# Kernel optimization log

Measured on AMD Instinct MI355X. Metric: run time of the kernel, lower is better.

## Reference

```python
import jax, jax.numpy as jnp
import numpy as np
from jax import lax

B, DIM, H, W = 16, 256, 64, 64
NH, KD = 8, 16
NH_KD = NH * KD        # 128
DH = 2 * NH_KD         # 256 (attn_ratio=2)
SCALE = KD ** -0.5
PE_LEN = 16


def conv1x1(x, Wt, b):
    # x: [B,Cin,H,W], Wt: [Cout,Cin]
    return jnp.einsum('oi,bihw->bohw', Wt, x) + b[None, :, None, None]


def dwconv3x3(x, Wt, b):
    # depthwise 3x3, pad 1. Wt: [C,1,3,3]
    C = x.shape[1]
    y = lax.conv_general_dilated(x, Wt, window_strides=(1, 1),
                                 padding=((1, 1), (1, 1)),
                                 feature_group_count=C,
                                 dimension_numbers=('NCHW', 'OIHW', 'NCHW'))
    return y + b[None, :, None, None]


def relu6(x):
    return jnp.clip(x, 0.0, 6.0)


def h_sigmoid(x):
    return jnp.clip(x + 3.0, 0.0, 6.0) / 6.0


def interp_linear(pe, N):
    # F.interpolate(mode='linear', align_corners=False). pe: [1,C,S] -> [1,C,N]
    S = pe.shape[-1]
    src = (jnp.arange(N, dtype=jnp.float32) + 0.5) * (S / N) - 0.5
    src = jnp.clip(src, 0.0, S - 1.0)
    lo = jnp.floor(src).astype(jnp.int32)
    hi = jnp.minimum(lo + 1, S - 1)
    w = (src - lo.astype(jnp.float32))[None, None, :]
    return pe[..., lo] * (1.0 - w) + pe[..., hi] * w


def axial_attn(qm, km, vm, pe_q, pe_k, N):
    # qm,km: [B,NH_KD,N] squeezed q/k means; vm: [B,DH,N]
    qn = (qm + interp_linear(pe_q, N)).reshape(B, NH, KD, N).transpose(0, 1, 3, 2)  # [B,h,N,kd]
    kn = (km + interp_linear(pe_k, N)).reshape(B, NH, KD, N)                        # [B,h,kd,N]
    vn = vm.reshape(B, NH, DH // NH, N).transpose(0, 1, 3, 2)                       # [B,h,N,d]
    attn = jax.nn.softmax(jnp.einsum('bhik,bhkj->bhij', qn, kn) * SCALE, axis=-1)
    xx = jnp.einsum('bhij,bhjd->bhid', attn, vn)                                    # [B,h,N,d]
    return xx.transpose(0, 1, 3, 2).reshape(B, DH, N)


def reference(x, Wq, bq, Wk, bk, Wv, bv, W_dw, b_dw, W_pw, b_pw,
              W_row, b_row, W_col, b_col, W_proj, b_proj,
              pe_rowq, pe_rowk, pe_colq, pe_colk):
    q = conv1x1(x, Wq, bq)   # [B,NH_KD,H,W]
    k = conv1x1(x, Wk, bk)   # [B,NH_KD,H,W]
    v = conv1x1(x, Wv, bv)   # [B,DH,H,W]

    qkv = jnp.concatenate([q, k, v], axis=1)        # [B,2*DH,H,W]
    qkv = relu6(dwconv3x3(qkv, W_dw, b_dw))
    qkv = conv1x1(qkv, W_pw, b_pw)                  # [B,DIM,H,W]

    # row attention (squeeze over W)
    xx_row = axial_attn(q.mean(-1), k.mean(-1), v.mean(-1), pe_rowq, pe_rowk, H)
    xx_row = conv1x1(relu6(xx_row[..., None]), W_row, b_row)          # [B,DH,H,1]

    # column attention (squeeze over H)
    xx_col = axial_attn(q.mean(-2), k.mean(-2), v.mean(-2), pe_colq, pe_colk, W)
    xx_col = conv1x1(relu6(xx_col[:, :, None, :]), W_col, b_col)      # [B,DH,1,W]

    xx = v + (xx_row + xx_col)                      # broadcast to [B,DH,H,W]
    xx = conv1x1(relu6(xx), W_proj, b_proj)         # [B,DIM,H,W]
    return h_sigmoid(xx) * qkv


def setup_inputs() -> dict:
    key = jax.random.key(0)
    ks = iter(jax.random.split(key, 32))

    def n(shape, fan_in=None):
        s = 1.0 if fan_in is None else 1.0 / np.sqrt(fan_in)
        return jax.random.normal(next(ks), shape, jnp.float32) * s

    return {
        'x': n((B, DIM, H, W)),
        'Wq': n((NH_KD, DIM), DIM), 'bq': n((NH_KD,), DIM),
        'Wk': n((NH_KD, DIM), DIM), 'bk': n((NH_KD,), DIM),
        'Wv': n((DH, DIM), DIM), 'bv': n((DH,), DIM),
        'W_dw': n((2 * DH, 1, 3, 3), 9), 'b_dw': n((2 * DH,), 9),
        'W_pw': n((DIM, 2 * DH), 2 * DH), 'b_pw': n((DIM,), 2 * DH),
        'W_row': n((DH, DH), DH), 'b_row': n((DH,), DH),
        'W_col': n((DH, DH), DH), 'b_col': n((DH,), DH),
        'W_proj': n((DIM, DH), DH), 'b_proj': n((DIM,), DH),
        'pe_rowq': n((1, NH_KD, PE_LEN)), 'pe_rowk': n((1, NH_KD, PE_LEN)),
        'pe_colq': n((1, NH_KD, PE_LEN)), 'pe_colk': n((1, NH_KD, PE_LEN)),
    }
```

## Files before the change

kernel.cpp:

```cpp
#include <hip/hip_runtime.h>


typedef short s16x8 __attribute__((ext_vector_type(8)));
typedef short s16x4 __attribute__((ext_vector_type(4)));
typedef float f32x4 __attribute__((ext_vector_type(4)));

#define OFF_QKVS 0ULL
#define OFF_DWO  67108864ULL
#define OFF_XBF  167772160ULL
#define OFF_MR   201326592ULL
#define OFF_MC   203423744ULL
#define OFF_XXA  205520896ULL
#define OFF_XRCT 207618048ULL
#define OFF_WQKV 209715200ULL
#define OFF_WPW  209977344ULL
#define OFF_WPR  210239488ULL
#define OFF_BQKV 210370560ULL

__device__ __forceinline__ float bf2f(unsigned short u) {
  unsigned int x = ((unsigned int)u) << 16;
  return __builtin_bit_cast(float, x);
}
__device__ __forceinline__ unsigned short f2bf(float f) {
  unsigned int x = __builtin_bit_cast(unsigned int, f);
  x += 0x7fffu + ((x >> 16) & 1u);
  return (unsigned short)(x >> 16);
}
__device__ __forceinline__ float relu6f(float v) { return fminf(fmaxf(v, 0.f), 6.f); }

__device__ __forceinline__ void mfma16(f32x4& d, s16x8 a, s16x8 b) {
  asm("v_mfma_f32_16x16x32_bf16 %0, %1, %2, %0" : "+v"(d) : "v"(a), "v"(b));
}

__global__ __launch_bounds__(256) void pack_k(
    const float* __restrict__ Wq, const float* __restrict__ Wk, const float* __restrict__ Wv,
    const float* __restrict__ bq, const float* __restrict__ bk, const float* __restrict__ bv,
    const float* __restrict__ Wpw, const float* __restrict__ Wpr,
    unsigned short* __restrict__ wqkv, unsigned short* __restrict__ wpw,
    unsigned short* __restrict__ wpr, float* __restrict__ bqkv)
{
  const int i = blockIdx.x * 256 + threadIdx.x;
  if (i < 131072) {
    const int o = i >> 8, k = i & 255;
    float v = (o < 128) ? Wq[o * 256 + k]
            : (o < 256) ? Wk[(o - 128) * 256 + k]
                        : Wv[(o - 256) * 256 + k];
    wqkv[i] = f2bf(v);
  } else if (i < 262144) {
    const int j = i - 131072;
    wpw[j] = f2bf(Wpw[j]);
  } else if (i < 327680) {
    const int j = i - 262144;
    wpr[j] = f2bf(Wpr[j]);
  } else if (i < 328192) {
    const int o = i - 327680;
    bqkv[o] = (o < 128) ? bq[o] : (o < 256) ? bk[o - 128] : bv[o - 256];
  }
}

__global__ __launch_bounds__(256) void xt_k(const float* __restrict__ x,
                                            unsigned short* __restrict__ xbf)
{
  __shared__ float tile[64][68];
  const int bid = blockIdx.x;
  const int nt = bid & 63, ct = (bid >> 6) & 3, b = bid >> 8;
  const int n0 = nt * 64, c0 = ct * 64;
  const int tid = threadIdx.x;
  #pragma unroll
  for (int p = 0; p < 4; ++p) {
    const int g = tid + p * 256;
    const int row = g >> 4, ch = g & 15;
    const float4 v = *(const float4*)&x[((size_t)b * 256 + c0 + row) * 4096 + n0 + ch * 4];
    *(float4*)&tile[row][ch * 4] = v;
  }
  __syncthreads();
  #pragma unroll
  for (int p = 0; p < 2; ++p) {
    const int g = tid + p * 256;
    const int nr = g >> 3, cc = g & 7;
    s16x8 o;
    #pragma unroll
    for (int q = 0; q < 8; ++q) o[q] = f2bf(tile[cc * 8 + q][nr]);
    *(s16x8*)&xbf[((size_t)b * 4096 + n0 + nr) * 256 + c0 + cc * 8] = o;
  }
}

template <int ROWS>
__device__ __forceinline__ void stage_rows(const unsigned short* __restrict__ src,
                                           int ld, unsigned short (*S)[72], int tid)
{
  #pragma unroll
  for (int p = 0; p < ROWS / 32; ++p) {
    const int g = tid + p * 256;
    const int r = g >> 3, sl = g & 7;
    *(s16x8*)&S[r][sl * 8] = *(const s16x8*)&src[(size_t)r * ld + sl * 8];
  }
}

__device__ __forceinline__ void compute64(const unsigned short (*As)[72],
                                          const unsigned short (*Xs)[72],
                                          f32x4 (*acc)[2], int wm, int wn, int lane)
{
  #pragma unroll
  for (int ks = 0; ks < 64; ks += 32) {
    s16x8 bF[2], aF[8];
    #pragma unroll
    for (int j = 0; j < 2; ++j)
      bF[j] = *(const s16x8*)&Xs[wn * 32 + j * 16 + (lane & 15)][ks + (lane >> 4) * 8];
    #pragma unroll
    for (int i = 0; i < 8; ++i)
      aF[i] = *(const s16x8*)&As[wm * 128 + i * 16 + (lane & 15)][ks + (lane >> 4) * 8];
    #pragma unroll
    for (int i = 0; i < 8; ++i)
      #pragma unroll
      for (int j = 0; j < 2; ++j)
        mfma16(acc[i][j], aF[i], bF[j]);
  }
}

__global__ __launch_bounds__(256, 2) void qkv_k(
    const unsigned short* __restrict__ wqkv, const float* __restrict__ bias,
    const unsigned short* __restrict__ xbf, unsigned short* __restrict__ qkvs,
    float* __restrict__ mr)
{
  __shared__ __align__(16) unsigned short As[256][72];
  __shared__ __align__(16) unsigned short Xs[64][72];
  __shared__ float msum[2][256];
  const int tid = threadIdx.x, lane = tid & 63, wave = tid >> 6;
  const int wm = wave >> 1, wn = wave & 1;
  const int bid = blockIdx.x;
  const int nt = bid & 63, mt = (bid >> 6) & 1, b = bid >> 7;
  const int row0 = mt * 256, col0 = nt * 64;

  const unsigned short* Abase = wqkv + (size_t)row0 * 256;
  const unsigned short* Xbase = xbf + ((size_t)b * 4096 + col0) * 256;

  f32x4 acc[8][2];
  #pragma unroll
  for (int i = 0; i < 8; ++i)
    #pragma unroll
    for (int j = 0; j < 2; ++j) acc[i][j] = (f32x4){0.f, 0.f, 0.f, 0.f};

  s16x8 pA[8], pX[2];
  #pragma unroll
  for (int p = 0; p < 8; ++p) {
    const int g = tid + p * 256, r = g >> 3, sl = g & 7;
    pA[p] = *(const s16x8*)&Abase[(size_t)r * 256 + sl * 8];
  }
  #pragma unroll
  for (int p = 0; p < 2; ++p) {
    const int g = tid + p * 256, r = g >> 3, sl = g & 7;
    pX[p] = *(const s16x8*)&Xbase[(size_t)r * 256 + sl * 8];
  }

  for (int k0 = 0; k0 < 256; k0 += 64) {
    #pragma unroll
    for (int p = 0; p < 8; ++p) {
      const int g = tid + p * 256, r = g >> 3, sl = g & 7;
      *(s16x8*)&As[r][sl * 8] = pA[p];
    }
    #pragma unroll
    for (int p = 0; p < 2; ++p) {
      const int g = tid + p * 256, r = g >> 3, sl = g & 7;
      *(s16x8*)&Xs[r][sl * 8] = pX[p];
    }
    __syncthreads();
    if (k0 + 64 < 256) {
      const int kn = k0 + 64;
      #pragma unroll
      for (int p = 0; p < 8; ++p) {
        const int g = tid + p * 256, r = g >> 3, sl = g & 7;
        pA[p] = *(const s16x8*)&Abase[(size_t)r * 256 + kn + sl * 8];
      }
      #pragma unroll
      for (int p = 0; p < 2; ++p) {
        const int g = tid + p * 256, r = g >> 3, sl = g & 7;
        pX[p] = *(const s16x8*)&Xbase[(size_t)r * 256 + kn + sl * 8];
      }
    }
    compute64(As, Xs, acc, wm, wn, lane);
    __syncthreads();
  }

  #pragma unroll
  for (int i = 0; i < 8; ++i) {
    const int o0 = row0 + wm * 128 + i * 16 + ((lane >> 4) << 2);
    const float4 b4 = *(const float4*)&bias[o0];
    #pragma unroll
    for (int j = 0; j < 2; ++j) {
      const int n = col0 + wn * 32 + j * 16 + (lane & 15);
      s16x4 pk;
      pk[0] = f2bf(acc[i][j][0] + b4.x);
      pk[1] = f2bf(acc[i][j][1] + b4.y);
      pk[2] = f2bf(acc[i][j][2] + b4.z);
      pk[3] = f2bf(acc[i][j][3] + b4.w);
      *(s16x4*)&qkvs[((size_t)b * 4096 + n) * 512 + o0] = pk;
    }
    #pragma unroll
    for (int r = 0; r < 4; ++r) {
      float s = acc[i][0][r] + acc[i][1][r];
      s += __shfl_xor(s, 1);
      s += __shfl_xor(s, 2);
      s += __shfl_xor(s, 4);
      s += __shfl_xor(s, 8);
      if ((lane & 15) == 0)
        msum[wn][wm * 128 + i * 16 + ((lane >> 4) << 2) + r] = s;
    }
  }
  __syncthreads();
  mr[((size_t)b * 512 + row0 + tid) * 64 + nt] =
      (msum[0][tid] + msum[1][tid]) * (1.f / 64.f) + bias[row0 + tid];
}

__global__ __launch_bounds__(256) void mc_k(const unsigned short* __restrict__ qkvs,
                                            float* __restrict__ mc)
{
  const int bid = blockIdx.x;
  const int pos = bid & 63, b = bid >> 6;
  const int c = threadIdx.x * 2;
  float s0 = 0.f, s1 = 0.f;
  for (int t = 0; t < 64; ++t) {
    const int n = t * 64 + pos;
    const unsigned u = *(const unsigned*)&qkvs[((size_t)b * 4096 + n) * 512 + c];
    s0 += bf2f((unsigned short)u);
    s1 += bf2f((unsigned short)(u >> 16));
  }
  mc[((size_t)b * 512 + c) * 64 + pos] = s0 * (1.f / 64.f);
  mc[((size_t)b * 512 + c + 1) * 64 + pos] = s1 * (1.f / 64.f);
}

__global__ __launch_bounds__(512, 2) void dwm_k(
    const unsigned short* __restrict__ qkvs, const float* __restrict__ Wdw,
    const float* __restrict__ bdw, unsigned short* __restrict__ dwo)
{
  const int bid = blockIdx.x;
  const int h = bid & 63, b = bid >> 6;
  const int tid = threadIdx.x;
  const int c0 = (tid & 63) * 8;
  const int w0 = (tid >> 6) * 8;
  float w9[8][9], bs[8];
  #pragma unroll
  for (int q = 0; q < 8; ++q) {
    bs[q] = bdw[c0 + q];
    #pragma unroll
    for (int j = 0; j < 9; ++j) w9[q][j] = Wdw[(c0 + q) * 9 + j];
  }
  float acc[8][8];
  #pragma unroll
  for (int w = 0; w < 8; ++w)
    #pragma unroll
    for (int q = 0; q < 8; ++q) acc[w][q] = bs[q];

  const size_t base = (size_t)b * 4096 * 512;
  #pragma unroll
  for (int dr = 0; dr < 3; ++dr) {
    const int hh = h + dr - 1;
    if ((unsigned)hh < 64u) {
      s16x8 rowd[10];
      #pragma unroll
      for (int t = 0; t < 10; ++t) {
        const int ww = w0 + t - 1;
        if ((unsigned)ww < 64u)
          rowd[t] = *(const s16x8*)&qkvs[base + (size_t)(hh * 64 + ww) * 512 + c0];
        else
          rowd[t] = (s16x8){0, 0, 0, 0, 0, 0, 0, 0};
      }
      #pragma unroll
      for (int t = 0; t < 10; ++t) {
        float fv[8];
        #pragma unroll
        for (int q = 0; q < 8; ++q) fv[q] = bf2f((unsigned short)rowd[t][q]);
        #pragma unroll
        for (int dc = 0; dc < 3; ++dc) {
          const int w = t - dc;
          if (w >= 0 && w < 8) {
            #pragma unroll
            for (int q = 0; q < 8; ++q)
              acc[w][q] += w9[q][dr * 3 + dc] * fv[q];
          }
        }
      }
    }
  }
  #pragma unroll
  for (int w = 0; w < 8; ++w) {
    s16x8 o8;
    #pragma unroll
    for (int q = 0; q < 8; ++q) o8[q] = f2bf(relu6f(acc[w][q]));
    *(s16x8*)&dwo[base + (size_t)(h * 64 + w0 + w) * 512 + c0] = o8;
  }
}

__global__ __launch_bounds__(256, 2) void fin_k(
    const unsigned short* __restrict__ wpw, const float* __restrict__ bpw,
    const unsigned short* __restrict__ wpr, const float* __restrict__ bpr,
    const unsigned short* __restrict__ dwo, const unsigned short* __restrict__ qkvs,
    const float* __restrict__ xrct, float* __restrict__ out)
{
  __shared__ __align__(16) unsigned short As[256][72];
  __shared__ __align__(16) unsigned short Xs[64][72];
  const int tid = threadIdx.x, lane = tid & 63, wave = tid >> 6;
  const int wm = wave >> 1, wn = wave & 1;
  const int bid = blockIdx.x;
  const int nt = bid & 63, b = bid >> 6;
  const int col0 = nt * 64;

  f32x4 apw[8][2], apr[8][2];
  #pragma unroll
  for (int i = 0; i < 8; ++i)
    #pragma unroll
    for (int j = 0; j < 2; ++j) {
      apw[i][j] = (f32x4){0.f, 0.f, 0.f, 0.f};
      apr[i][j] = (f32x4){0.f, 0.f, 0.f, 0.f};
    }

  const unsigned short* Xb1 = dwo + ((size_t)b * 4096 + col0) * 512;
  s16x8 pX[2];
  #pragma unroll
  for (int p = 0; p < 2; ++p) {
    const int g = tid + p * 256, r = g >> 3, sl = g & 7;
    pX[p] = *(const s16x8*)&Xb1[(size_t)r * 512 + sl * 8];
  }
  for (int k0 = 0; k0 < 512; k0 += 64) {
    stage_rows<256>(wpw + k0, 512, As, tid);
    #pragma unroll
    for (int p = 0; p < 2; ++p) {
      const int g = tid + p * 256, r = g >> 3, sl = g & 7;
      *(s16x8*)&Xs[r][sl * 8] = pX[p];
    }
    __syncthreads();
    if (k0 + 64 < 512) {
      const int kn = k0 + 64;
      #pragma unroll
      for (int p = 0; p < 2; ++p) {
        const int g = tid + p * 256, r = g >> 3, sl = g & 7;
        pX[p] = *(const s16x8*)&Xb1[(size_t)r * 512 + kn + sl * 8];
      }
    }
    compute64(As, Xs, apw, wm, wn, lane);
    __syncthreads();
  }

  const float* xr = &xrct[(((size_t)b * 2 + 0) * 64 + nt) * 256];
  const float* xc = &xrct[(((size_t)b * 2 + 1) * 64) * 256];
  const unsigned short* Vb = qkvs + ((size_t)b * 4096 + col0) * 512 + 256;
  s16x8 pV[2];
  #pragma unroll
  for (int p = 0; p < 2; ++p) {
    const int g = tid + p * 256, r = g >> 3, sl = g & 7;
    pV[p] = *(const s16x8*)&Vb[(size_t)r * 512 + sl * 8];
  }
  for (int k0 = 0; k0 < 256; k0 += 64) {
    stage_rows<256>(wpr + k0, 256, As, tid);
    #pragma unroll
    for (int p = 0; p < 2; ++p) {
      const int g = tid + p * 256, r = g >> 3, sl = g & 7;
      const int kk = k0 + sl * 8;
      const float4 a0 = *(const float4*)&xr[kk];
      const float4 a1 = *(const float4*)&xr[kk + 4];
      const float4 c0v = *(const float4*)&xc[(size_t)r * 256 + kk];
      const float4 c1v = *(const float4*)&xc[(size_t)r * 256 + kk + 4];
      const float ar[8] = {a0.x, a0.y, a0.z, a0.w, a1.x, a1.y, a1.z, a1.w};
      const float ac[8] = {c0v.x, c0v.y, c0v.z, c0v.w, c1v.x, c1v.y, c1v.z, c1v.w};
      s16x8 o;
      #pragma unroll
      for (int q = 0; q < 8; ++q)
        o[q] = f2bf(relu6f(bf2f((unsigned short)pV[p][q]) + ar[q] + ac[q]));
      *(s16x8*)&Xs[r][sl * 8] = o;
    }
    __syncthreads();
    if (k0 + 64 < 256) {
      const int kn = k0 + 64;
      #pragma unroll
      for (int p = 0; p < 2; ++p) {
        const int g = tid + p * 256, r = g >> 3, sl = g & 7;
        pV[p] = *(const s16x8*)&Vb[(size_t)r * 512 + kn + sl * 8];
      }
    }
    compute64(As, Xs, apr, wm, wn, lane);
    __syncthreads();
  }

  #pragma unroll
  for (int i = 0; i < 8; ++i) {
    const int o0 = wm * 128 + i * 16 + ((lane >> 4) << 2);
    const float4 bw = *(const float4*)&bpw[o0];
    const float4 bp = *(const float4*)&bpr[o0];
    const float bwv[4] = {bw.x, bw.y, bw.z, bw.w};
    const float bpv[4] = {bp.x, bp.y, bp.z, bp.w};
    #pragma unroll
    for (int j = 0; j < 2; ++j) {
      const int n = col0 + wn * 32 + j * 16 + (lane & 15);
      #pragma unroll
      for (int r = 0; r < 4; ++r) {
        const float hs = fminf(fmaxf(apr[i][j][r] + bpv[r] + 3.f, 0.f), 6.f) * (1.f / 6.f);
        out[((size_t)b * 256 + o0 + r) * 4096 + n] = hs * (apw[i][j][r] + bwv[r]);
      }
    }
  }
}

__global__ __launch_bounds__(256) void attn_k(
    const float* __restrict__ mr, const float* __restrict__ mc,
    const float* __restrict__ pe_rq, const float* __restrict__ pe_rk,
    const float* __restrict__ pe_cq, const float* __restrict__ pe_ck,
    float* __restrict__ xxa)
{
  __shared__ float qh[16][69], kh[16][69], vh[32][69], P[64][69];
  const int bid = blockIdx.x;
  const int hd = bid & 7, axis = (bid >> 3) & 1, b = bid >> 4;
  const float* m  = axis ? mc : mr;
  const float* pq = axis ? pe_cq : pe_rq;
  const float* pk = axis ? pe_ck : pe_rk;
  const int tid = threadIdx.x;

  #pragma unroll
  for (int p = 0; p < 4; ++p) {
    const int e = tid + p * 256;
    const int kd = e >> 6, i = e & 63;
    float srcp = 0.25f * (float)i - 0.375f;
    srcp = fminf(fmaxf(srcp, 0.f), 15.f);
    const int lo = (int)srcp;
    const int hi = min(lo + 1, 15);
    const float w = srcp - (float)lo;
    const int cq = hd * 16 + kd;
    qh[kd][i] = m[((size_t)b * 512 + cq) * 64 + i]
              + pq[cq * 16 + lo] * (1.f - w) + pq[cq * 16 + hi] * w;
    kh[kd][i] = m[((size_t)b * 512 + 128 + cq) * 64 + i]
              + pk[cq * 16 + lo] * (1.f - w) + pk[cq * 16 + hi] * w;
  }
  #pragma unroll
  for (int p = 0; p < 8; ++p) {
    const int e = tid + p * 256;
    const int d = e >> 6, j = e & 63;
    vh[d][j] = m[((size_t)b * 512 + 256 + hd * 32 + d) * 64 + j];
  }
  __syncthreads();
  {
    const int i = tid >> 2, j0 = (tid & 3) * 16;
    float qr[16];
    #pragma unroll
    for (int kd = 0; kd < 16; ++kd) qr[kd] = qh[kd][i];
    #pragma unroll
    for (int jj = 0; jj < 16; ++jj) {
      float s = 0.f;
      #pragma unroll
      for (int kd = 0; kd < 16; ++kd) s += qr[kd] * kh[kd][j0 + jj];
      P[i][j0 + jj] = s * 0.25f;
    }
  }
  __syncthreads();
  if (tid < 64) {
    float mx = -1e30f;
    for (int j = 0; j < 64; ++j) mx = fmaxf(mx, P[tid][j]);
    float sum = 0.f;
    for (int j = 0; j < 64; ++j) { const float e = __expf(P[tid][j] - mx); P[tid][j] = e; sum += e; }
    const float inv = 1.f / sum;
    for (int j = 0; j < 64; ++j) P[tid][j] *= inv;
  }
  __syncthreads();
  #pragma unroll
  for (int p = 0; p < 8; ++p) {
    const int e = tid + p * 256;
    const int d = e >> 6, i = e & 63;
    float s = 0.f;
    for (int j = 0; j < 64; ++j) s += P[i][j] * vh[d][j];
    xxa[(((size_t)(b * 2 + axis)) * 256 + hd * 32 + d) * 64 + i] = s;
  }
}

__global__ __launch_bounds__(256) void rc_k(
    const float* __restrict__ xxa, const float* __restrict__ Wrow, const float* __restrict__ brow,
    const float* __restrict__ Wcol, const float* __restrict__ bcol, float* __restrict__ xrct)
{
  __shared__ float stf[256][8];
  const int bid = blockIdx.x;
  const int ic = bid & 7, axis = (bid >> 3) & 1, b = bid >> 4;
  const float* W  = axis ? Wcol : Wrow;
  const float* bi = axis ? bcol : brow;
  const int tid = threadIdx.x;
  {
    const float* srcp = xxa + (((size_t)(b * 2 + axis)) * 256 + tid) * 64 + ic * 8;
    #pragma unroll
    for (int q = 0; q < 8; ++q) stf[tid][q] = relu6f(srcp[q]);
  }
  __syncthreads();
  float acc[8] = {0.f, 0.f, 0.f, 0.f, 0.f, 0.f, 0.f, 0.f};
  for (int c = 0; c < 256; ++c) {
    const float w = W[tid * 256 + c];
    const float4 s0 = *(const float4*)&stf[c][0];
    const float4 s1 = *(const float4*)&stf[c][4];
    acc[0] += w * s0.x; acc[1] += w * s0.y; acc[2] += w * s0.z; acc[3] += w * s0.w;
    acc[4] += w * s1.x; acc[5] += w * s1.y; acc[6] += w * s1.z; acc[7] += w * s1.w;
  }
  const float bb = bi[tid];
  #pragma unroll
  for (int q = 0; q < 8; ++q)
    xrct[(((size_t)(b * 2 + axis)) * 64 + ic * 8 + q) * 256 + tid] = acc[q] + bb;
}

extern "C" void kernel_launch(void* const* d_in, const int* in_sizes, int n_in,
                              void* d_out, int out_size, void* d_ws, size_t ws_size,
                              hipStream_t stream)
{
  const float* x    = (const float*)d_in[0];
  const float* Wq   = (const float*)d_in[1];
  const float* bq   = (const float*)d_in[2];
  const float* Wk   = (const float*)d_in[3];
  const float* bk   = (const float*)d_in[4];
  const float* Wv   = (const float*)d_in[5];
  const float* bv   = (const float*)d_in[6];
  const float* Wdw  = (const float*)d_in[7];
  const float* bdw  = (const float*)d_in[8];
  const float* Wpw  = (const float*)d_in[9];
  const float* bpw  = (const float*)d_in[10];
  const float* Wrow = (const float*)d_in[11];
  const float* brow = (const float*)d_in[12];
  const float* Wcol = (const float*)d_in[13];
  const float* bcol = (const float*)d_in[14];
  const float* Wpr  = (const float*)d_in[15];
  const float* bpr  = (const float*)d_in[16];
  const float* perq = (const float*)d_in[17];
  const float* perk = (const float*)d_in[18];
  const float* pecq = (const float*)d_in[19];
  const float* peck = (const float*)d_in[20];

  char* ws = (char*)d_ws;
  unsigned short* qkvs = (unsigned short*)(ws + OFF_QKVS);
  unsigned short* dwo  = (unsigned short*)(ws + OFF_DWO);
  unsigned short* xbf  = (unsigned short*)(ws + OFF_XBF);
  float* mr   = (float*)(ws + OFF_MR);
  float* mc   = (float*)(ws + OFF_MC);
  float* xxa  = (float*)(ws + OFF_XXA);
  float* xrct = (float*)(ws + OFF_XRCT);
  unsigned short* wqkv = (unsigned short*)(ws + OFF_WQKV);
  unsigned short* wpw  = (unsigned short*)(ws + OFF_WPW);
  unsigned short* wpr  = (unsigned short*)(ws + OFF_WPR);
  float* bqkv = (float*)(ws + OFF_BQKV);

  pack_k<<<1282, 256, 0, stream>>>(Wq, Wk, Wv, bq, bk, bv, Wpw, Wpr, wqkv, wpw, wpr, bqkv);
  xt_k<<<4096, 256, 0, stream>>>(x, xbf);

  qkv_k<<<2048, 256, 0, stream>>>(wqkv, bqkv, xbf, qkvs, mr);
  dwm_k<<<1024, 512, 0, stream>>>(qkvs, Wdw, bdw, dwo);
  mc_k<<<1024, 256, 0, stream>>>(qkvs, mc);
  attn_k<<<256, 256, 0, stream>>>(mr, mc, perq, perk, pecq, peck, xxa);
  rc_k<<<256, 256, 0, stream>>>(xxa, Wrow, brow, Wcol, bcol, xrct);
  fin_k<<<1024, 256, 0, stream>>>(wpw, bpw, wpr, bpr, dwo, qkvs, xrct, (float*)d_out);
}
```

Measured before the change: 215.7 us.

## Halve GEMM M-tiles in qkv and fin kernels, stage qkv output via LDS

The qkv and fin GEMM kernels shrink their output-row tile from 256 to 128 and double the grid. This lowers accumulator register use and LDS footprint, which should raise occupancy. The qkv kernel also drops its register prefetch pipeline in favour of direct staging, and it transposes the output through shared memory so global stores are coalesced 16-byte row writes instead of scattered 8-byte ones. The cost is that each fin block now reloads its dwo/v activation tile for both M halves, and the xrct relu work is duplicated as well.

```diff
diff --git a/kernel.cpp b/kernel.cpp
--- a/kernel.cpp
+++ b/kernel.cpp
@@ -97,21 +97,22 @@
   }
 }
 
+template <int MI>
 __device__ __forceinline__ void compute64(const unsigned short (*As)[72],
                                           const unsigned short (*Xs)[72],
                                           f32x4 (*acc)[2], int wm, int wn, int lane)
 {
   #pragma unroll
   for (int ks = 0; ks < 64; ks += 32) {
-    s16x8 bF[2], aF[8];
+    s16x8 bF[2], aF[MI];
     #pragma unroll
     for (int j = 0; j < 2; ++j)
       bF[j] = *(const s16x8*)&Xs[wn * 32 + j * 16 + (lane & 15)][ks + (lane >> 4) * 8];
     #pragma unroll
-    for (int i = 0; i < 8; ++i)
-      aF[i] = *(const s16x8*)&As[wm * 128 + i * 16 + (lane & 15)][ks + (lane >> 4) * 8];
-    #pragma unroll
-    for (int i = 0; i < 8; ++i)
+    for (int i = 0; i < MI; ++i)
+      aF[i] = *(const s16x8*)&As[wm * (MI * 16) + i * 16 + (lane & 15)][ks + (lane >> 4) * 8];
+    #pragma unroll
+    for (int i = 0; i < MI; ++i)
       #pragma unroll
       for (int j = 0; j < 2; ++j)
         mfma16(acc[i][j], aF[i], bF[j]);
@@ -123,78 +124,43 @@
     const unsigned short* __restrict__ xbf, unsigned short* __restrict__ qkvs,
     float* __restrict__ mr)
 {
-  __shared__ __align__(16) unsigned short As[256][72];
+  __shared__ __align__(16) unsigned short As[128][72];
   __shared__ __align__(16) unsigned short Xs[64][72];
-  __shared__ float msum[2][256];
+  __shared__ float msum[2][128];
   const int tid = threadIdx.x, lane = tid & 63, wave = tid >> 6;
   const int wm = wave >> 1, wn = wave & 1;
   const int bid = blockIdx.x;
-  const int nt = bid & 63, mt = (bid >> 6) & 1, b = bid >> 7;
-  const int row0 = mt * 256, col0 = nt * 64;
-
-  const unsigned short* Abase = wqkv + (size_t)row0 * 256;
-  const unsigned short* Xbase = xbf + ((size_t)b * 4096 + col0) * 256;
-
-  f32x4 acc[8][2];
-  #pragma unroll
-  for (int i = 0; i < 8; ++i)
+  const int nt = bid & 63, mt = (bid >> 6) & 3, b = bid >> 8;
+  const int row0 = mt * 128, col0 = nt * 64;
+
+  f32x4 acc[4][2];
+  #pragma unroll
+  for (int i = 0; i < 4; ++i)
     #pragma unroll
     for (int j = 0; j < 2; ++j) acc[i][j] = (f32x4){0.f, 0.f, 0.f, 0.f};
 
-  s16x8 pA[8], pX[2];
-  #pragma unroll
-  for (int p = 0; p < 8; ++p) {
-    const int g = tid + p * 256, r = g >> 3, sl = g & 7;
-    pA[p] = *(const s16x8*)&Abase[(size_t)r * 256 + sl * 8];
-  }
-  #pragma unroll
-  for (int p = 0; p < 2; ++p) {
-    const int g = tid + p * 256, r = g >> 3, sl = g & 7;
-    pX[p] = *(const s16x8*)&Xbase[(size_t)r * 256 + sl * 8];
-  }
-
   for (int k0 = 0; k0 < 256; k0 += 64) {
-    #pragma unroll
-    for (int p = 0; p < 8; ++p) {
-      const int g = tid + p * 256, r = g >> 3, sl = g & 7;
-      *(s16x8*)&As[r][sl * 8] = pA[p];
-    }
-    #pragma unroll
-    for (int p = 0; p < 2; ++p) {
-      const int g = tid + p * 256, r = g >> 3, sl = g & 7;
-      *(s16x8*)&Xs[r][sl * 8] = pX[p];
-    }
+    stage_rows<128>(wqkv + (size_t)row0 * 256 + k0, 256, As, tid);
+    stage_rows<64>(xbf + ((size_t)b * 4096 + col0) * 256 + k0, 256, Xs, tid);
     __syncthreads();
-    if (k0 + 64 < 256) {
-      const int kn = k0 + 64;
-      #pragma unroll
-      for (int p = 0; p < 8; ++p) {
-        const int g = tid + p * 256, r = g >> 3, sl = g & 7;
-        pA[p] = *(const s16x8*)&Abase[(size_t)r * 256 + kn + sl * 8];
-      }
-      #pragma unroll
-      for (int p = 0; p < 2; ++p) {
-        const int g = tid + p * 256, r = g >> 3, sl = g & 7;
-        pX[p] = *(const s16x8*)&Xbase[(size_t)r * 256 + kn + sl * 8];
-      }
-    }
-    compute64(As, Xs, acc, wm, wn, lane);
+    compute64<4>(As, Xs, acc, wm, wn, lane);
     __syncthreads();
   }
 
-  #pragma unroll
-  for (int i = 0; i < 8; ++i) {
-    const int o0 = row0 + wm * 128 + i * 16 + ((lane >> 4) << 2);
-    const float4 b4 = *(const float4*)&bias[o0];
+  unsigned short (*Cs)[132] = (unsigned short (*)[132])As;
+  #pragma unroll
+  for (int i = 0; i < 4; ++i) {
+    const int ol = wm * 64 + i * 16 + ((lane >> 4) << 2);
+    const float4 b4 = *(const float4*)&bias[row0 + ol];
     #pragma unroll
     for (int j = 0; j < 2; ++j) {
-      const int n = col0 + wn * 32 + j * 16 + (lane & 15);
+      const int nl = wn * 32 + j * 16 + (lane & 15);
       s16x4 pk;
       pk[0] = f2bf(acc[i][j][0] + b4.x);
       pk[1] = f2bf(acc[i][j][1] + b4.y);
       pk[2] = f2bf(acc[i][j][2] + b4.z);
       pk[3] = f2bf(acc[i][j][3] + b4.w);
-      *(s16x4*)&qkvs[((size_t)b * 4096 + n) * 512 + o0] = pk;
+      *(s16x4*)&Cs[nl][ol] = pk;
     }
     #pragma unroll
     for (int r = 0; r < 4; ++r) {
@@ -203,13 +169,20 @@
       s += __shfl_xor(s, 2);
       s += __shfl_xor(s, 4);
       s += __shfl_xor(s, 8);
-      if ((lane & 15) == 0)
-        msum[wn][wm * 128 + i * 16 + ((lane >> 4) << 2) + r] = s;
+      if ((lane & 15) == 0) msum[wn][ol + r] = s;
     }
   }
   __syncthreads();
-  mr[((size_t)b * 512 + row0 + tid) * 64 + nt] =
-      (msum[0][tid] + msum[1][tid]) * (1.f / 64.f) + bias[row0 + tid];
+  #pragma unroll
+  for (int p = 0; p < 4; ++p) {
+    const int g = tid + p * 256;
+    const int nl = g >> 4, sl = g & 15;
+    *(s16x8*)&qkvs[((size_t)b * 4096 + col0 + nl) * 512 + row0 + sl * 8] =
+        *(const s16x8*)&Cs[nl][sl * 8];
+  }
+  if (tid < 128)
+    mr[((size_t)b * 512 + row0 + tid) * 64 + nt] =
+        (msum[0][tid] + msum[1][tid]) * (1.f / 64.f) + bias[row0 + tid];
 }
 
 __global__ __launch_bounds__(256) void mc_k(const unsigned short* __restrict__ qkvs,
@@ -297,17 +270,17 @@
     const unsigned short* __restrict__ dwo, const unsigned short* __restrict__ qkvs,
     const float* __restrict__ xrct, float* __restrict__ out)
 {
-  __shared__ __align__(16) unsigned short As[256][72];
+  __shared__ __align__(16) unsigned short As[128][72];
   __shared__ __align__(16) unsigned short Xs[64][72];
   const int tid = threadIdx.x, lane = tid & 63, wave = tid >> 6;
   const int wm = wave >> 1, wn = wave & 1;
   const int bid = blockIdx.x;
-  const int nt = bid & 63, b = bid >> 6;
-  const int col0 = nt * 64;
-
-  f32x4 apw[8][2], apr[8][2];
-  #pragma unroll
-  for (int i = 0; i < 8; ++i)
+  const int nt = bid & 63, mt = (bid >> 6) & 1, b = bid >> 7;
+  const int row0 = mt * 128, col0 = nt * 64;
+
+  f32x4 apw[4][2], apr[4][2];
+  #pragma unroll
+  for (int i = 0; i < 4; ++i)
     #pragma unroll
     for (int j = 0; j < 2; ++j) {
       apw[i][j] = (f32x4){0.f, 0.f, 0.f, 0.f};
@@ -322,7 +295,7 @@
     pX[p] = *(const s16x8*)&Xb1[(size_t)r * 512 + sl * 8];
   }
   for (int k0 = 0; k0 < 512; k0 += 64) {
-    stage_rows<256>(wpw + k0, 512, As, tid);
+    stage_rows<128>(wpw + (size_t)row0 * 512 + k0, 512, As, tid);
     #pragma unroll
     for (int p = 0; p < 2; ++p) {
       const int g = tid + p * 256, r = g >> 3, sl = g & 7;
@@ -337,7 +310,7 @@
         pX[p] = *(const s16x8*)&Xb1[(size_t)r * 512 + kn + sl * 8];
       }
     }
-    compute64(As, Xs, apw, wm, wn, lane);
+    compute64<4>(As, Xs, apw, wm, wn, lane);
     __syncthreads();
   }
 
@@ -351,7 +324,7 @@
     pV[p] = *(const s16x8*)&Vb[(size_t)r * 512 + sl * 8];
   }
   for (int k0 = 0; k0 < 256; k0 += 64) {
-    stage_rows<256>(wpr + k0, 256, As, tid);
+    stage_rows<128>(wpr + (size_t)row0 * 256 + k0, 256, As, tid);
     #pragma unroll
     for (int p = 0; p < 2; ++p) {
       const int g = tid + p * 256, r = g >> 3, sl = g & 7;
@@ -377,13 +350,13 @@
         pV[p] = *(const s16x8*)&Vb[(size_t)r * 512 + kn + sl * 8];
       }
     }
-    compute64(As, Xs, apr, wm, wn, lane);
+    compute64<4>(As, Xs, apr, wm, wn, lane);
     __syncthreads();
   }
 
   #pragma unroll
-  for (int i = 0; i < 8; ++i) {
-    const int o0 = wm * 128 + i * 16 + ((lane >> 4) << 2);
+  for (int i = 0; i < 4; ++i) {
+    const int o0 = row0 + wm * 64 + i * 16 + ((lane >> 4) << 2);
     const float4 bw = *(const float4*)&bpw[o0];
     const float4 bp = *(const float4*)&bpr[o0];
     const float bwv[4] = {bw.x, bw.y, bw.z, bw.w};
@@ -541,10 +514,10 @@
   pack_k<<<1282, 256, 0, stream>>>(Wq, Wk, Wv, bq, bk, bv, Wpw, Wpr, wqkv, wpw, wpr, bqkv);
   xt_k<<<4096, 256, 0, stream>>>(x, xbf);
 
-  qkv_k<<<2048, 256, 0, stream>>>(wqkv, bqkv, xbf, qkvs, mr);
+  qkv_k<<<4096, 256, 0, stream>>>(wqkv, bqkv, xbf, qkvs, mr);
   dwm_k<<<1024, 512, 0, stream>>>(qkvs, Wdw, bdw, dwo);
   mc_k<<<1024, 256, 0, stream>>>(qkvs, mc);
   attn_k<<<256, 256, 0, stream>>>(mr, mc, perq, perk, pecq, peck, xxa);
   rc_k<<<256, 256, 0, stream>>>(xxa, Wrow, brow, Wcol, bcol, xrct);
-  fin_k<<<1024, 256, 0, stream>>>(wpw, bpw, wpr, bpr, dwo, qkvs, xrct, (float*)d_out);
-}
+  fin_k<<<2048, 256, 0, stream>>>(wpw, bpw, wpr, bpr, dwo, qkvs, xrct, (float*)d_out);
+}
```

Result: slower. 225.8 us (+4.7%).

## Keep QKV weight slice resident in LDS and stream X tiles per block

Applied to the files above, without the earlier changes.

The QKV projection kernel now loads a 128x256 weight slice into shared memory once per block, using an XOR-swizzled layout, and loops over 512 spatial columns in 128-column tiles. It prefetches X chunks through registers. The old version reloaded a 256-row weight tile every K step for each 64-column tile. The change cuts repeated weight traffic and launch count (2048 to 512 blocks), and the swizzle targets LDS bank conflicts. The risks are lower occupancy from 80KB of LDS per block and fewer blocks to fill the GPU. The row means are now written directly per 64-column half without a shared reduction.

```diff
diff --git a/kernel.cpp b/kernel.cpp
--- a/kernel.cpp
+++ b/kernel.cpp
@@ -123,93 +123,108 @@
     const unsigned short* __restrict__ xbf, unsigned short* __restrict__ qkvs,
     float* __restrict__ mr)
 {
-  __shared__ __align__(16) unsigned short As[256][72];
-  __shared__ __align__(16) unsigned short Xs[64][72];
-  __shared__ float msum[2][256];
+  __shared__ __align__(16) unsigned short Ws[128][256];
+  __shared__ __align__(16) unsigned short Xs[128][64];
   const int tid = threadIdx.x, lane = tid & 63, wave = tid >> 6;
   const int wm = wave >> 1, wn = wave & 1;
   const int bid = blockIdx.x;
-  const int nt = bid & 63, mt = (bid >> 6) & 1, b = bid >> 7;
-  const int row0 = mt * 256, col0 = nt * 64;
-
-  const unsigned short* Abase = wqkv + (size_t)row0 * 256;
-  const unsigned short* Xbase = xbf + ((size_t)b * 4096 + col0) * 256;
-
-  f32x4 acc[8][2];
-  #pragma unroll
-  for (int i = 0; i < 8; ++i)
-    #pragma unroll
-    for (int j = 0; j < 2; ++j) acc[i][j] = (f32x4){0.f, 0.f, 0.f, 0.f};
-
-  s16x8 pA[8], pX[2];
-  #pragma unroll
-  for (int p = 0; p < 8; ++p) {
-    const int g = tid + p * 256, r = g >> 3, sl = g & 7;
-    pA[p] = *(const s16x8*)&Abase[(size_t)r * 256 + sl * 8];
-  }
-  #pragma unroll
-  for (int p = 0; p < 2; ++p) {
-    const int g = tid + p * 256, r = g >> 3, sl = g & 7;
-    pX[p] = *(const s16x8*)&Xbase[(size_t)r * 256 + sl * 8];
-  }
-
-  for (int k0 = 0; k0 < 256; k0 += 64) {
-    #pragma unroll
-    for (int p = 0; p < 8; ++p) {
-      const int g = tid + p * 256, r = g >> 3, sl = g & 7;
-      *(s16x8*)&As[r][sl * 8] = pA[p];
-    }
-    #pragma unroll
-    for (int p = 0; p < 2; ++p) {
-      const int g = tid + p * 256, r = g >> 3, sl = g & 7;
-      *(s16x8*)&Xs[r][sl * 8] = pX[p];
-    }
-    __syncthreads();
-    if (k0 + 64 < 256) {
-      const int kn = k0 + 64;
-      #pragma unroll
-      for (int p = 0; p < 8; ++p) {
-        const int g = tid + p * 256, r = g >> 3, sl = g & 7;
-        pA[p] = *(const s16x8*)&Abase[(size_t)r * 256 + kn + sl * 8];
-      }
-      #pragma unroll
-      for (int p = 0; p < 2; ++p) {
-        const int g = tid + p * 256, r = g >> 3, sl = g & 7;
-        pX[p] = *(const s16x8*)&Xbase[(size_t)r * 256 + kn + sl * 8];
-      }
-    }
-    compute64(As, Xs, acc, wm, wn, lane);
-    __syncthreads();
-  }
-
-  #pragma unroll
-  for (int i = 0; i < 8; ++i) {
-    const int o0 = row0 + wm * 128 + i * 16 + ((lane >> 4) << 2);
-    const float4 b4 = *(const float4*)&bias[o0];
-    #pragma unroll
-    for (int j = 0; j < 2; ++j) {
-      const int n = col0 + wn * 32 + j * 16 + (lane & 15);
-      s16x4 pk;
-      pk[0] = f2bf(acc[i][j][0] + b4.x);
-      pk[1] = f2bf(acc[i][j][1] + b4.y);
-      pk[2] = f2bf(acc[i][j][2] + b4.z);
-      pk[3] = f2bf(acc[i][j][3] + b4.w);
-      *(s16x4*)&qkvs[((size_t)b * 4096 + n) * 512 + o0] = pk;
-    }
-    #pragma unroll
-    for (int r = 0; r < 4; ++r) {
-      float s = acc[i][0][r] + acc[i][1][r];
-      s += __shfl_xor(s, 1);
-      s += __shfl_xor(s, 2);
-      s += __shfl_xor(s, 4);
-      s += __shfl_xor(s, 8);
-      if ((lane & 15) == 0)
-        msum[wn][wm * 128 + i * 16 + ((lane >> 4) << 2) + r] = s;
-    }
-  }
-  __syncthreads();
-  mr[((size_t)b * 512 + row0 + tid) * 64 + nt] =
-      (msum[0][tid] + msum[1][tid]) * (1.f / 64.f) + bias[row0 + tid];
+  const int ng = bid & 7, mt = (bid >> 3) & 3, b = bid >> 5;
+  const int row0 = mt * 128;
+  const int n_base = ng * 512;
+  const unsigned short* Xb = xbf + ((size_t)b * 4096 + n_base) * 256;
+
+  s16x8 pX[4];
+  #pragma unroll
+  for (int p = 0; p < 4; ++p) {
+    const int g = tid + p * 256, r = g >> 3, gl = g & 7;
+    pX[p] = *(const s16x8*)&Xb[(size_t)r * 256 + gl * 8];
+  }
+  #pragma unroll
+  for (int p = 0; p < 16; ++p) {
+    const int g = tid + p * 256;
+    const int r = g >> 5, gl = g & 31;
+    *(s16x8*)&Ws[r][(gl ^ (r & 7)) * 8] =
+        *(const s16x8*)&wqkv[(size_t)(row0 + r) * 256 + gl * 8];
+  }
+
+  for (int t = 0; t < 4; ++t) {
+    f32x4 acc[4][4];
+    #pragma unroll
+    for (int i = 0; i < 4; ++i)
+      #pragma unroll
+      for (int j = 0; j < 4; ++j) acc[i][j] = (f32x4){0.f, 0.f, 0.f, 0.f};
+
+    #pragma unroll
+    for (int c = 0; c < 4; ++c) {
+      __syncthreads();
+      #pragma unroll
+      for (int p = 0; p < 4; ++p) {
+        const int g = tid + p * 256, r = g >> 3, gl = g & 7;
+        *(s16x8*)&Xs[r][(gl ^ (r & 7)) * 8] = pX[p];
+      }
+      __syncthreads();
+      const int ci = t * 4 + c;
+      if (ci < 15) {
+        const int tn = (ci + 1) >> 2, cn = (ci + 1) & 3;
+        #pragma unroll
+        for (int p = 0; p < 4; ++p) {
+          const int g = tid + p * 256, r = g >> 3, gl = g & 7;
+          pX[p] = *(const s16x8*)&Xb[(size_t)(tn * 128 + r) * 256 + cn * 64 + gl * 8];
+        }
+      }
+      #pragma unroll
+      for (int ks = 0; ks < 64; ks += 32) {
+        s16x8 aF[4], bF[4];
+        #pragma unroll
+        for (int i = 0; i < 4; ++i) {
+          const int row = wm * 64 + i * 16 + (lane & 15);
+          const int kg = ((c * 64 + ks) >> 3) + (lane >> 4);
+          aF[i] = *(const s16x8*)&Ws[row][(kg ^ (row & 7)) * 8];
+        }
+        #pragma unroll
+        for (int j = 0; j < 4; ++j) {
+          const int row = wn * 64 + j * 16 + (lane & 15);
+          const int kg = (ks >> 3) + (lane >> 4);
+          bF[j] = *(const s16x8*)&Xs[row][(kg ^ (row & 7)) * 8];
+        }
+        #pragma unroll
+        for (int i = 0; i < 4; ++i)
+          #pragma unroll
+          for (int j = 0; j < 4; ++j)
+            mfma16(acc[i][j], aF[i], bF[j]);
+      }
+    }
+
+    const int n0 = n_base + t * 128;
+    #pragma unroll
+    for (int i = 0; i < 4; ++i) {
+      const int o0 = row0 + wm * 64 + i * 16 + ((lane >> 4) << 2);
+      const float4 b4 = *(const float4*)&bias[o0];
+      const float bv[4] = {b4.x, b4.y, b4.z, b4.w};
+      #pragma unroll
+      for (int j = 0; j < 4; ++j) {
+        const int n = n0 + wn * 64 + j * 16 + (lane & 15);
+        s16x4 pk;
+        pk[0] = f2bf(acc[i][j][0] + bv[0]);
+        pk[1] = f2bf(acc[i][j][1] + bv[1]);
+        pk[2] = f2bf(acc[i][j][2] + bv[2]);
+        pk[3] = f2bf(acc[i][j][3] + bv[3]);
+        *(s16x4*)&qkvs[((size_t)b * 4096 + n) * 512 + o0] = pk;
+      }
+      #pragma unroll
+      for (int r = 0; r < 4; ++r) {
+        float s = acc[i][0][r] + acc[i][1][r] + acc[i][2][r] + acc[i][3][r];
+        s += __shfl_xor(s, 1);
+        s += __shfl_xor(s, 2);
+        s += __shfl_xor(s, 4);
+        s += __shfl_xor(s, 8);
+        if ((lane & 15) == 0) {
+          const int o = o0 + r;
+          mr[((size_t)b * 512 + o) * 64 + (n0 >> 6) + wn] = s * (1.f / 64.f) + bv[r];
+        }
+      }
+    }
+  }
 }
 
 __global__ __launch_bounds__(256) void mc_k(const unsigned short* __restrict__ qkvs,
@@ -541,7 +556,7 @@
   pack_k<<<1282, 256, 0, stream>>>(Wq, Wk, Wv, bq, bk, bv, Wpw, Wpr, wqkv, wpw, wpr, bqkv);
   xt_k<<<4096, 256, 0, stream>>>(x, xbf);
 
-  qkv_k<<<2048, 256, 0, stream>>>(wqkv, bqkv, xbf, qkvs, mr);
+  qkv_k<<<512, 256, 0, stream>>>(wqkv, bqkv, xbf, qkvs, mr);
   dwm_k<<<1024, 512, 0, stream>>>(qkvs, Wdw, bdw, dwo);
   mc_k<<<1024, 256, 0, stream>>>(qkvs, mc);
   attn_k<<<256, 256, 0, stream>>>(mr, mc, perq, perk, pecq, peck, xxa);
```

Result: faster. 209.9 us (-2.7%).
